# Optimization experiments

Hardware: AMD Instinct MI355X
Metric: run time of the kernel (lower is better)

The kernel has to match this reference:

```python
import jax, jax.numpy as jnp
import numpy as np

N, E, D, C, L, G = 50000, 1600000, 128, 10, 4, 512
BN_EPS = 1e-5


def setup_inputs() -> dict:
    key = jax.random.key(0)
    ks = jax.random.split(key, 16)
    s = 0.05  # weight init scale
    inp = {
        "x": jax.random.normal(ks[0], (N, D), dtype=jnp.float32),
        "edge_index": jax.random.randint(ks[1], (2, E), 0, N, dtype=jnp.int32),
        "batch": jnp.sort(jax.random.randint(ks[2], (N,), 0, G, dtype=jnp.int32)),
        "num_graphs": G,
        # GINConv inner MLP params (layer 0 input dim == D since num_features == num_hidden)
        "conv_W1": jax.random.normal(ks[3], (L, D, D), dtype=jnp.float32) * s,
        "conv_b1": jnp.zeros((L, D), dtype=jnp.float32),
        "conv_bn_g": jnp.ones((L, D), dtype=jnp.float32),
        "conv_bn_b": jnp.zeros((L, D), dtype=jnp.float32),
        "conv_W2": jax.random.normal(ks[4], (L, D, D), dtype=jnp.float32) * s,
        "conv_b2": jnp.zeros((L, D), dtype=jnp.float32),
        # outer BatchNorm after each conv
        "bn_g": jnp.ones((L, D), dtype=jnp.float32),
        "bn_b": jnp.zeros((L, D), dtype=jnp.float32),
        # per-scale classifier heads (L+1 of them; fcs[0] input dim == num_features == D)
        "fc_W": jax.random.normal(ks[5], (L + 1, D, C), dtype=jnp.float32) * s,
        "fc_b": jnp.zeros((L + 1, C), dtype=jnp.float32),
    }
    return inp


def _bn(h, g, b):
    # BatchNorm1d in training mode: batch stats over nodes, biased variance
    m = h.mean(axis=0)
    v = jnp.mean((h - m) ** 2, axis=0)
    return (h - m) * jax.lax.rsqrt(v + BN_EPS) * g + b


def reference(x, edge_index, batch, num_graphs, conv_W1, conv_b1, conv_bn_g,
              conv_bn_b, conv_W2, conv_b2, bn_g, bn_b, fc_W, fc_b):
    n_nodes = x.shape[0]
    src, dst = edge_index[0], edge_index[1]
    outs = [x]
    h = x
    for i in range(L):
        # GINConv (eps=0, aggr='add'): mlp(x + scatter_add of neighbor features)
        agg = jax.ops.segment_sum(h[src], dst, num_segments=n_nodes)  # [N, D]
        z = h + agg
        z = z @ conv_W1[i] + conv_b1[i]
        z = jax.nn.relu(_bn(z, conv_bn_g[i], conv_bn_b[i]))
        z = z @ conv_W2[i] + conv_b2[i]
        h = jax.nn.relu(_bn(z, bn_g[i], bn_b[i]))
        outs.append(h)
    out = None
    for i, o in enumerate(outs):
        pooled = jax.ops.segment_sum(o, batch, num_segments=num_graphs)  # [G, D]
        logits = pooled @ fc_W[i] + fc_b[i]
        out = logits if out is None else out + logits
    return jax.nn.log_softmax(out, axis=-1)
```

## Files before the change

kernel.cpp:

```cpp
#include <hip/hip_runtime.h>

#define NN 50000
#define EE 1600000
#define DD 128
#define CC 10
#define LLAY 4
#define GG 512
#define GD (GG*DD)
#define NB 196
#define BK_EDGES 1024
#define BUCKCAP 16000
#define NSUB 16
#define SUBW 3125
#define WPAD 136

static constexpr float BN_EPS = 1e-5f;
static constexpr float INV_N = 1.0f / (float)NN;

typedef __bf16 bf16x8 __attribute__((ext_vector_type(8)));
typedef float f32x4 __attribute__((ext_vector_type(4)));

static __device__ __forceinline__ float bflo(unsigned u){ return __uint_as_float(u << 16); }
static __device__ __forceinline__ float bfhi(unsigned u){ return __uint_as_float(u & 0xffff0000u); }
static __device__ __forceinline__ unsigned short f2bf(float f){
    unsigned u = __float_as_uint(f);
    return (unsigned short)((u + 0x7fffu + ((u >> 16) & 1u)) >> 16);
}
static __device__ __forceinline__ unsigned packbf(float a, float b){
    return (unsigned)f2bf(a) | ((unsigned)f2bf(b) << 16);
}
static __device__ __forceinline__ unsigned encf(float f){
    unsigned b = __float_as_uint(f);
    return (b & 0x80000000u) ? ~b : (b | 0x80000000u);
}
static __device__ __forceinline__ float decf(unsigned e){
    unsigned b = (e & 0x80000000u) ? (e ^ 0x80000000u) : ~e;
    return __uint_as_float(b);
}
static __device__ __forceinline__ bf16x8 ldfrag(const unsigned short* p){
    union { uint4 u; bf16x8 b; } t; t.u = *(const uint4*)p; return t.b;
}
static __device__ __forceinline__ bf16x8 asfrag(uint4 u){
    union { uint4 u; bf16x8 b; } t; t.u = u; return t.b;
}


__global__ void zero_k(int* p, int n){
    int i = blockIdx.x * 256 + threadIdx.x;
    if (i < n) p[i] = 0;
}

__global__ void wprep_k(const float* __restrict__ W1, const float* __restrict__ W2,
                        unsigned short* __restrict__ Wtall){
    int idx = blockIdx.x * 256 + threadIdx.x;
    int mat = idx >> 14; int rr = idx & 16383;
    int k = rr >> 7; int j = rr & 127;
    const float* Wsrc = (mat < 4) ? (W1 + mat * 16384) : (W2 + (mat - 4) * 16384);
    Wtall[mat * 16384 + j * 128 + k] = f2bf(Wsrc[k * 128 + j]);
}

__global__ void gsearch_k(const int* __restrict__ batch, int* __restrict__ gstart){
    int g = blockIdx.x * 256 + threadIdx.x;
    if (g <= GG){
        int lo = 0, hi = NN;
        while (lo < hi){ int mid = (lo + hi) >> 1; if (batch[mid] < g) lo = mid + 1; else hi = mid; }
        gstart[g] = lo;
    }
}

__global__ __launch_bounds__(256) void binA_k(const int* __restrict__ srcA,
                                              const int* __restrict__ dstA,
                                              int* __restrict__ bucketCur,
                                              unsigned* __restrict__ binned){
    __shared__ int cnt[256];
    __shared__ int lb[256];
    __shared__ int bas[NB];
    __shared__ int off[NB];
    __shared__ unsigned stage[BK_EDGES];
    __shared__ int tots;
    int tid = threadIdx.x;
    cnt[tid] = 0;
    if (tid < NB) off[tid] = 0;
    __syncthreads();
    int e0 = blockIdx.x * BK_EDGES;
    int myB[4]; unsigned myVal[4];
    #pragma unroll
    for (int k = 0; k < 4; k++){
        int e = e0 + tid + k * 256;
        bool v = (e < EE);
        int d = v ? dstA[e] : -1;
        int s = v ? srcA[e] : 0;
        myB[k] = v ? (d >> 8) : -1;
        myVal[k] = (unsigned)s | ((unsigned)(d & 255) << 17);
        if (v) atomicAdd(&cnt[d >> 8], 1);
    }
    __syncthreads();
    int v = cnt[tid];
    lb[tid] = v; __syncthreads();
    for (int o = 1; o < 256; o <<= 1){
        int x = 0; if (tid >= o) x = lb[tid - o];
        __syncthreads(); lb[tid] += x; __syncthreads();
    }
    int incl = lb[tid];
    if (tid == 255) tots = incl;
    __syncthreads();
    lb[tid] = incl - v;
    if (tid < NB && v > 0) bas[tid] = atomicAdd(&bucketCur[tid], v);
    __syncthreads();
    #pragma unroll
    for (int k = 0; k < 4; k++){
        int b = myB[k];
        if (b >= 0){
            int p = lb[b] + atomicAdd(&off[b], 1);
            stage[p] = myVal[k];
        }
    }
    __syncthreads();
    int tot = tots;
    for (int i = tid; i < tot; i += 256){
        int lo = 0, hi = NB - 1;
        while (lo < hi){
            int mid = (lo + hi + 1) >> 1;
            if (lb[mid] <= i) lo = mid; else hi = mid - 1;
        }
        binned[lo * BUCKCAP + bas[lo] + (i - lb[lo])] = stage[i];
    }
}

__global__ __launch_bounds__(256) void bscan_k(const int* __restrict__ bucketCur,
                                               int* __restrict__ bucketBase,
                                               int* __restrict__ rp){
    __shared__ int lds[256];
    int t = threadIdx.x;
    int v = (t < NB) ? bucketCur[t] : 0;
    lds[t] = v; __syncthreads();
    for (int o = 1; o < 256; o <<= 1){
        int xv = 0; if (t >= o) xv = lds[t - o];
        __syncthreads(); lds[t] += xv; __syncthreads();
    }
    int excl = lds[t] - v;
    if (t < NB) bucketBase[t] = excl;
    if (t == 0){ bucketBase[NB] = EE; rp[NN] = EE; }
}

__global__ __launch_bounds__(1024) void binB_k(const unsigned* __restrict__ binned,
                                               const int* __restrict__ bucketCur,
                                               const int* __restrict__ bucketBase,
                                               int* __restrict__ rp,
                                               int* __restrict__ ssort){
    __shared__ int c16[256 * NSUB];
    __shared__ int b16[256 * NSUB];
    __shared__ int nt[256];
    int b = blockIdx.x, tid = threadIdx.x;
    int nb0 = b * 256;
    int nmax = NN - nb0; if (nmax > 256) nmax = 256;
    for (int i = tid; i < 256 * NSUB; i += 1024) c16[i] = 0;
    __syncthreads();
    int cntb = bucketCur[b];
    int src0 = b * BUCKCAP;
    int base = bucketBase[b];
    for (int i = tid; i < cntb; i += 1024){
        unsigned u = binned[src0 + i];
        int src = (int)(u & 0x1FFFFu); int dl = (int)(u >> 17);
        atomicAdd(&c16[dl * NSUB + src / SUBW], 1);
    }
    __syncthreads();
    int cc[NSUB]; int tot = 0;
    if (tid < 256){
        #pragma unroll
        for (int k = 0; k < NSUB; k++){ cc[k] = c16[tid * NSUB + k]; tot += cc[k]; }
        nt[tid] = tot;
    }
    __syncthreads();
    for (int o = 1; o < 256; o <<= 1){
        int xv = 0;
        if (tid < 256 && tid >= o) xv = nt[tid - o];
        __syncthreads();
        if (tid < 256) nt[tid] += xv;
        __syncthreads();
    }
    if (tid < 256){
        int p = base + nt[tid] - tot;
        if (tid < nmax) rp[nb0 + tid] = p;
        int run = p;
        #pragma unroll
        for (int k = 0; k < NSUB; k++){ b16[tid * NSUB + k] = run; run += cc[k]; }
    }
    __syncthreads();
    for (int i = tid; i < 256 * NSUB; i += 1024) c16[i] = 0;
    __syncthreads();
    for (int i = tid; i < cntb; i += 1024){
        unsigned u = binned[src0 + i];
        int src = (int)(u & 0x1FFFFu); int dl = (int)(u >> 17);
        int t = src / SUBW;
        int pos = b16[dl * NSUB + t] + atomicAdd(&c16[dl * NSUB + t], 1);
        ssort[pos] = src;
    }
}

__global__ __launch_bounds__(256) void xmax_k(const float* __restrict__ x,
                                              unsigned* __restrict__ xmaxE){
    __shared__ float sm[256];
    int tid = threadIdx.x;
    int col = tid & 127, rh = tid >> 7;
    float m = 0.f;
    for (int r = blockIdx.x * 2 + rh; r < NN; r += 1024)
        m = fmaxf(m, fabsf(x[r * 128 + col]));
    sm[tid] = m; __syncthreads();
    if (tid < 128){
        m = fmaxf(sm[tid], sm[tid + 128]);
        atomicMax(&xmaxE[col], __float_as_uint(m));
    }
}

__global__ void qx_k(const unsigned* __restrict__ xmaxE,
                     float* __restrict__ qD, float* __restrict__ qR){
    int c = threadIdx.x;
    float m = __uint_as_float(xmaxE[c]);
    qD[c] = m * (1.f / 127.f);
    qR[c] = (m > 0.f) ? 127.f / m : 0.f;
}

__global__ __launch_bounds__(256) void convxpool_k(const float2* __restrict__ x2,
                                                   const int* __restrict__ gstart,
                                                   unsigned short* __restrict__ h8u,
                                                   const float* __restrict__ qR0,
                                                   float* __restrict__ outp){
    __shared__ float sd[512];
    int b = blockIdx.x; int gid = b >> 2, chunk = b & 3;
    int tid = threadIdx.x; int c = tid & 63, rs = tid >> 6;
    int s = gstart[gid], e = gstart[gid + 1];
    float2 rv = ((const float2*)qR0)[c];
    float a0 = 0.f, a1 = 0.f;
    for (int n = s + chunk * 4 + rs; n < e; n += 16){
        float2 v = x2[n * 64 + c];
        int i0 = (int)rintf(v.x * rv.x) + 128; i0 = min(max(i0, 0), 255);
        int i1 = (int)rintf(v.y * rv.y) + 128; i1 = min(max(i1, 0), 255);
        h8u[n * 64 + c] = (unsigned short)(i0 | (i1 << 8));
        a0 += v.x; a1 += v.y;
    }
    sd[tid] = a0; sd[256 + tid] = a1; __syncthreads();
    if (tid < 64){
        float r0 = 0.f, r1 = 0.f;
        #pragma unroll
        for (int k2 = 0; k2 < 4; k2++){ r0 += sd[tid + 64 * k2]; r1 += sd[256 + tid + 64 * k2]; }
        atomicAdd(&outp[gid * 128 + 2 * tid], r0);
        atomicAdd(&outp[gid * 128 + 2 * tid + 1], r1);
    }
}


__global__ __launch_bounds__(256) void agg_k(const unsigned short* __restrict__ h8u,
                                             const int* __restrict__ rp,
                                             const int* __restrict__ ssort,
                                             const float* __restrict__ qD,
                                             float offv,
                                             unsigned* __restrict__ z32,
                                             float* __restrict__ zstats){
    int tid = threadIdx.x;
    if (blockIdx.x == 0) zstats[tid] = 0.f;
    int n = blockIdx.x * 4 + (tid >> 6);
    int lane = tid & 63;
    int e  = __builtin_amdgcn_readfirstlane(rp[n]);
    int e1 = __builtin_amdgcn_readfirstlane(rp[n + 1]);
    int deg = e1 - e;
    unsigned su = (unsigned)h8u[n * 64 + lane];
    unsigned acc0 = su & 0xFFu, acc1 = su >> 8;
    for (; e + 15 < e1; e += 16){
        int sA[16];
        #pragma unroll
        for (int k = 0; k < 16; k++) sA[k] = ssort[e + k];
        unsigned uA[16];
        #pragma unroll
        for (int k = 0; k < 16; k++) uA[k] = (unsigned)h8u[sA[k] * 64 + lane];
        #pragma unroll
        for (int k = 0; k < 16; k++){ acc0 += uA[k] & 0xFFu; acc1 += uA[k] >> 8; }
    }
    for (; e + 3 < e1; e += 4){
        int s0 = ssort[e], s1 = ssort[e + 1], s2 = ssort[e + 2], s3 = ssort[e + 3];
        unsigned u0 = (unsigned)h8u[s0 * 64 + lane];
        unsigned u1 = (unsigned)h8u[s1 * 64 + lane];
        unsigned u2 = (unsigned)h8u[s2 * 64 + lane];
        unsigned u3 = (unsigned)h8u[s3 * 64 + lane];
        acc0 += (u0 & 0xFFu) + (u1 & 0xFFu) + (u2 & 0xFFu) + (u3 & 0xFFu);
        acc1 += (u0 >> 8) + (u1 >> 8) + (u2 >> 8) + (u3 >> 8);
    }
    for (; e < e1; ++e){
        unsigned u0 = (unsigned)h8u[ssort[e] * 64 + lane];
        acc0 += u0 & 0xFFu; acc1 += u0 >> 8;
    }
    float2 qd = ((const float2*)qD)[lane];
    float degoff = offv * (float)(deg + 1);
    float z0 = qd.x * ((float)acc0 - degoff);
    float z1 = qd.y * ((float)acc1 - degoff);
    z32[n * 64 + lane] = packbf(z0, z1);
}

template<int TR>
__global__ __launch_bounds__(256) void gemm_k(const unsigned* __restrict__ A32,
                                              const unsigned short* __restrict__ Wtg,
                                              const float* __restrict__ bias,
                                              unsigned short* __restrict__ Cst,
                                              const float* __restrict__ stats,
                                              const float* __restrict__ gma,
                                              const float* __restrict__ bta,
                                              float* __restrict__ ostats,
                                              float* __restrict__ zstats,
                                              float* __restrict__ zpool,
                                              unsigned* __restrict__ mst){
    __shared__ __align__(16) unsigned short Wl[64 * WPAD];
    __shared__ float sred[1024];
    __shared__ __align__(16) float sl[128], tl[128];
    int tid = threadIdx.x;
    int slice = blockIdx.x & 1;
    int tileb = blockIdx.x >> 1;

    int wv = tid >> 6, lane = tid & 63;
    int rowbase = tileb * 64 + wv * 16;
    int r0 = rowbase + (lane & 15);
    int kd = (lane >> 4) * 4;
    uint4 va[4];
    #pragma unroll
    for (int ks = 0; ks < 4; ks++)
        va[ks] = (r0 < NN) ? *(const uint4*)(A32 + r0 * 64 + ks * 16 + kd) : make_uint4(0,0,0,0);

    if (blockIdx.x == 0 && zstats) zstats[tid] = 0.f;
    if (zpool && blockIdx.x < 256) zpool[blockIdx.x * 256 + tid] = 0.f;
    {
        const uint4* src = (const uint4*)(Wtg + slice * 64 * 128);
        uint4* dst = (uint4*)Wl;
        #pragma unroll
        for (int i = 0; i < 4; i++){
            int idx = tid + 256 * i;
            int row = idx >> 4, c16 = idx & 15;
            dst[row * (WPAD / 8) + c16] = src[idx];
        }
    }
    if (TR && tid < 128){
        float mean = stats[tid] * INV_N;
        float q    = stats[128 + tid] * INV_N;
        float inv  = rsqrtf(q - mean * mean + BN_EPS);
        float s    = gma[tid] * inv;
        sl[tid] = s; tl[tid] = bta[tid] - mean * s;
    }
    __syncthreads();

    if (TR){
        #pragma unroll
        for (int ks = 0; ks < 4; ks++){
            int q = ks * 8 + (lane >> 4) * 2;
            float4 sA = ((const float4*)sl)[q], sB = ((const float4*)sl)[q + 1];
            float4 tA = ((const float4*)tl)[q], tB = ((const float4*)tl)[q + 1];
            float fs[8] = {sA.x, sA.y, sA.z, sA.w, sB.x, sB.y, sB.z, sB.w};
            float ft[8] = {tA.x, tA.y, tA.z, tA.w, tB.x, tB.y, tB.z, tB.w};
            unsigned* pa = (unsigned*)&va[ks];
            #pragma unroll
            for (int c = 0; c < 4; c++){
                float f0 = fmaxf(bflo(pa[c]) * fs[2*c] + ft[2*c], 0.f);
                float f1 = fmaxf(bfhi(pa[c]) * fs[2*c+1] + ft[2*c+1], 0.f);
                pa[c] = packbf(f0, f1);
            }
        }
    }

    f32x4 acc[4];
    #pragma unroll
    for (int ct = 0; ct < 4; ct++) acc[ct] = (f32x4){0.f, 0.f, 0.f, 0.f};

    #pragma unroll
    for (int ks = 0; ks < 4; ks++){
        int wk = ks * 32 + (lane >> 4) * 8;
        bf16x8 a0 = asfrag(va[ks]);
        #pragma unroll
        for (int ct = 0; ct < 4; ++ct){
            bf16x8 b = ldfrag(&Wl[(ct * 16 + (lane & 15)) * WPAD + wk]);
            acc[ct] = __builtin_amdgcn_mfma_f32_16x16x32_bf16(a0, b, acc[ct], 0, 0, 0);
        }
    }

    int cl = lane & 15, rq = lane >> 4;
    float colS[4], colQ[4];
    #pragma unroll
    for (int ct = 0; ct < 4; ++ct){
        int col = slice * 64 + ct * 16 + cl;
        float bv = bias[col];
        float ps = 0.f, pq = 0.f;
        float vx = -3.4e38f, vn = -3.4e38f;
        #pragma unroll
        for (int rr2 = 0; rr2 < 4; ++rr2){
            int grow = rowbase + rq * 4 + rr2;
            if (grow < NN){
                float val = acc[ct][rr2] + bv;
                Cst[grow * 128 + col] = f2bf(val);
                ps += val; pq += val * val;
                if (TR){ vx = fmaxf(vx, val); vn = fmaxf(vn, -val); }
            }
        }
        ps += __shfl_xor(ps, 16); pq += __shfl_xor(pq, 16);
        ps += __shfl_xor(ps, 32); pq += __shfl_xor(pq, 32);
        colS[ct] = ps; colQ[ct] = pq;
        if (TR){
            vx = fmaxf(vx, __shfl_xor(vx, 16)); vx = fmaxf(vx, __shfl_xor(vx, 32));
            vn = fmaxf(vn, __shfl_xor(vn, 16)); vn = fmaxf(vn, __shfl_xor(vn, 32));
            if (rq == 0){
                sred[512 + wv * 64 + ct * 16 + cl] = vx;
                sred[768 + wv * 64 + ct * 16 + cl] = vn;
            }
        }
    }
    if (rq == 0){
        #pragma unroll
        for (int ct = 0; ct < 4; ++ct){
            sred[wv * 64 + ct * 16 + cl]       = colS[ct];
            sred[256 + wv * 64 + ct * 16 + cl] = colQ[ct];
        }
    }
    __syncthreads();
    if (tid < 64){
        float s1 = sred[tid] + sred[64 + tid] + sred[128 + tid] + sred[192 + tid];
        float s2 = sred[256 + tid] + sred[320 + tid] + sred[384 + tid] + sred[448 + tid];
        atomicAdd(&ostats[slice * 64 + tid], s1);
        atomicAdd(&ostats[128 + slice * 64 + tid], s2);
        if (TR){
            float mx = fmaxf(fmaxf(sred[512 + tid], sred[576 + tid]),
                             fmaxf(sred[640 + tid], sred[704 + tid]));
            float mn = fmaxf(fmaxf(sred[768 + tid], sred[832 + tid]),
                             fmaxf(sred[896 + tid], sred[960 + tid]));
            atomicMax(&mst[slice * 64 + tid], encf(mx));
            atomicMax(&mst[128 + slice * 64 + tid], encf(mn));
        }
    }
}

__global__ __launch_bounds__(256) void ewpool_k(const unsigned* __restrict__ z32,
                                                const float* __restrict__ stats,
                                                const float* __restrict__ g,
                                                const float* __restrict__ b,
                                                const int* __restrict__ gstart,
                                                unsigned short* __restrict__ h8u,
                                                const unsigned* __restrict__ mst,
                                                float* __restrict__ qDn,
                                                float* __restrict__ outp){
    __shared__ float sd[512];
    int blk = blockIdx.x; int gid = blk >> 2, chunk = blk & 3;
    int tid = threadIdx.x;
    int c = tid & 63, rs = tid >> 6;
    int c2 = c * 2;
    float m0 = stats[c2] * INV_N,     q0 = stats[128 + c2] * INV_N;
    float inv0 = rsqrtf(q0 - m0 * m0 + BN_EPS);
    float s0 = g[c2] * inv0, t0 = b[c2] - m0 * s0;
    float m1 = stats[c2 + 1] * INV_N, q1 = stats[129 + c2] * INV_N;
    float inv1 = rsqrtf(q1 - m1 * m1 + BN_EPS);
    float s1 = g[c2 + 1] * inv1, t1 = b[c2 + 1] - m1 * s1;
    float zx0 = decf(mst[c2]),      zn0 = -decf(mst[128 + c2]);
    float zx1 = decf(mst[c2 + 1]),  zn1 = -decf(mst[129 + c2]);
    float hm0 = fmaxf(fmaxf(s0 * zx0 + t0, s0 * zn0 + t0), 0.f);
    float hm1 = fmaxf(fmaxf(s1 * zx1 + t1, s1 * zn1 + t1), 0.f);
    float r80 = (hm0 > 0.f) ? 255.f / hm0 : 0.f;
    float r81 = (hm1 > 0.f) ? 255.f / hm1 : 0.f;
    if (blk == 0 && rs == 0){
        qDn[c2]     = hm0 * (1.f / 255.f);
        qDn[c2 + 1] = hm1 * (1.f / 255.f);
    }
    int s = gstart[gid], e = gstart[gid + 1];
    float a0 = 0.f, a1 = 0.f;
    int n = s + chunk * 4 + rs;
    for (; n + 16 < e; n += 32){
        unsigned u0 = z32[n * 64 + c];
        unsigned u1 = z32[(n + 16) * 64 + c];
        float f0 = fmaxf(bflo(u0) * s0 + t0, 0.f);
        float f1 = fmaxf(bfhi(u0) * s1 + t1, 0.f);
        unsigned cu0 = (unsigned)(f0 * r80 + 0.5f); if (cu0 > 255u) cu0 = 255u;
        unsigned cu1 = (unsigned)(f1 * r81 + 0.5f); if (cu1 > 255u) cu1 = 255u;
        h8u[n * 64 + c] = (unsigned short)(cu0 | (cu1 << 8));
        a0 += f0; a1 += f1;
        f0 = fmaxf(bflo(u1) * s0 + t0, 0.f);
        f1 = fmaxf(bfhi(u1) * s1 + t1, 0.f);
        cu0 = (unsigned)(f0 * r80 + 0.5f); if (cu0 > 255u) cu0 = 255u;
        cu1 = (unsigned)(f1 * r81 + 0.5f); if (cu1 > 255u) cu1 = 255u;
        h8u[(n + 16) * 64 + c] = (unsigned short)(cu0 | (cu1 << 8));
        a0 += f0; a1 += f1;
    }
    for (; n < e; n += 16){
        unsigned u = z32[n * 64 + c];
        float f0 = fmaxf(bflo(u) * s0 + t0, 0.f);
        float f1 = fmaxf(bfhi(u) * s1 + t1, 0.f);
        unsigned cu0 = (unsigned)(f0 * r80 + 0.5f); if (cu0 > 255u) cu0 = 255u;
        unsigned cu1 = (unsigned)(f1 * r81 + 0.5f); if (cu1 > 255u) cu1 = 255u;
        h8u[n * 64 + c] = (unsigned short)(cu0 | (cu1 << 8));
        a0 += f0; a1 += f1;
    }
    sd[tid] = a0; sd[256 + tid] = a1; __syncthreads();
    if (tid < 64){
        float r0 = 0.f, r1 = 0.f;
        #pragma unroll
        for (int k2 = 0; k2 < 4; k2++){ r0 += sd[tid + 64 * k2]; r1 += sd[256 + tid + 64 * k2]; }
        atomicAdd(&outp[gid * 128 + 2 * tid], r0);
        atomicAdd(&outp[gid * 128 + 2 * tid + 1], r1);
    }
}

__global__ __launch_bounds__(64) void final_k(const float* __restrict__ pooled,
                                              const float* __restrict__ fcW,
                                              const float* __restrict__ fcb,
                                              float* __restrict__ out){
    int g = blockIdx.x, l = threadIdx.x;
    float p0[5], p1[5];
    #pragma unroll
    for (int i = 0; i < 5; i++){
        p0[i] = pooled[i * GD + g * 128 + l];
        p1[i] = pooled[i * GD + g * 128 + 64 + l];
    }
    float lg[10];
    #pragma unroll
    for (int c2 = 0; c2 < 10; c2++){
        float s = 0;
        #pragma unroll
        for (int i = 0; i < 5; i++){
            s += p0[i] * fcW[(i * 128 + l) * 10 + c2];
            s += p1[i] * fcW[(i * 128 + 64 + l) * 10 + c2];
        }
        #pragma unroll
        for (int off = 32; off >= 1; off >>= 1) s += __shfl_down(s, off);
        lg[c2] = s;
    }
    if (l == 0){
        #pragma unroll
        for (int c2 = 0; c2 < 10; c2++){
            float bs = 0;
            #pragma unroll
            for (int i = 0; i < 5; i++) bs += fcb[i * 10 + c2];
            lg[c2] += bs;
        }
        float mx = lg[0];
        #pragma unroll
        for (int c2 = 1; c2 < 10; c2++) mx = fmaxf(mx, lg[c2]);
        float se = 0;
        #pragma unroll
        for (int c2 = 0; c2 < 10; c2++) se += expf(lg[c2] - mx);
        float lse = mx + logf(se);
        #pragma unroll
        for (int c2 = 0; c2 < 10; c2++) out[g * 10 + c2] = lg[c2] - lse;
    }
}


extern "C" void kernel_launch(void* const* d_in, const int* in_sizes, int n_in,
                              void* d_out, int out_size, void* d_ws, size_t ws_size,
                              hipStream_t stream){
    (void)in_sizes; (void)n_in; (void)out_size; (void)ws_size;
    const float* x     = (const float*)d_in[0];
    const int*   ei    = (const int*)d_in[1];
    const int*   batch = (const int*)d_in[2];
    const float* cW1   = (const float*)d_in[4];
    const float* cb1   = (const float*)d_in[5];
    const float* cbng  = (const float*)d_in[6];
    const float* cbnb  = (const float*)d_in[7];
    const float* cW2   = (const float*)d_in[8];
    const float* cb2   = (const float*)d_in[9];
    const float* bng   = (const float*)d_in[10];
    const float* bnb   = (const float*)d_in[11];
    const float* fcW   = (const float*)d_in[12];
    const float* fcb   = (const float*)d_in[13];

    char* base = (char*)d_ws;
    size_t off = 0;
    auto alloc = [&](size_t bytes) -> void* {
        void* p = base + off;
        off = (off + bytes + 255) & ~(size_t)255;
        return p;
    };
    unsigned*       zA     = (unsigned*)alloc((size_t)NN * 64 * 4);
    unsigned*       zB     = (unsigned*)alloc((size_t)NN * 64 * 4);
    unsigned short* h8     = (unsigned short*)alloc((size_t)NN * 64 * 2);
    unsigned short* Wtall  = (unsigned short*)alloc(8 * 16384 * 2);
    int*            ssort  = (int*)alloc((size_t)EE * 4);
    int*            rp     = (int*)alloc((NN + 1) * 4);
    int*            gstart = (int*)alloc((GG + 1) * 4);
    int*            bucketBase = (int*)alloc((NB + 1) * 4);
    int*            bucketCur  = (int*)alloc(NB * 4);
    unsigned*       xmaxE  = (unsigned*)alloc(128 * 4);
    unsigned*       mstats = (unsigned*)alloc((size_t)LLAY * 256 * 4);
    float*          pooled = (float*)alloc((size_t)5 * GD * 4);
    float*          stats1 = (float*)alloc(256 * 4);
    float*          stats2 = (float*)alloc(256 * 4);
    float*          qD     = (float*)alloc(5 * 128 * 4);
    float*          qR     = (float*)alloc(128 * 4);
    unsigned*       binned = (unsigned*)zB;

    int zwords = (int)(((char*)(pooled + GD) - (char*)bucketCur) / 4);

    zero_k<<<(zwords + 255) / 256, 256, 0, stream>>>(bucketCur, zwords);
    wprep_k<<<512, 256, 0, stream>>>(cW1, cW2, Wtall);
    gsearch_k<<<3, 256, 0, stream>>>(batch, gstart);
    binA_k<<<(EE + BK_EDGES - 1) / BK_EDGES, 256, 0, stream>>>(ei, ei + EE, bucketCur, binned);
    bscan_k<<<1, 256, 0, stream>>>(bucketCur, bucketBase, rp);
    binB_k<<<NB, 1024, 0, stream>>>(binned, bucketCur, bucketBase, rp, ssort);
    xmax_k<<<512, 256, 0, stream>>>(x, xmaxE);
    qx_k<<<1, 128, 0, stream>>>(xmaxE, qD, qR);
    convxpool_k<<<4 * GG, 256, 0, stream>>>((const float2*)x, gstart, h8, qR, pooled);

    const int gemmGrid = 2 * ((NN + 63) / 64);
    for (int i = 0; i < LLAY; i++){
        agg_k<<<NN / 4, 256, 0, stream>>>(h8, rp, ssort,
                                          qD + i * 128, (i == 0) ? 128.f : 0.f, zA, stats1);
        gemm_k<0><<<gemmGrid, 256, 0, stream>>>(zA, Wtall + i * 16384, cb1 + i * 128,
                                                (unsigned short*)zB,
                                                nullptr, nullptr, nullptr, stats1, stats2,
                                                nullptr, nullptr);
        gemm_k<1><<<gemmGrid, 256, 0, stream>>>(zB, Wtall + (4 + i) * 16384, cb2 + i * 128,
                                                (unsigned short*)zA,
                                                stats1, cbng + i * 128, cbnb + i * 128, stats2,
                                                nullptr, pooled + (size_t)(i + 1) * GD,
                                                mstats + (size_t)i * 256);
        ewpool_k<<<4 * GG, 256, 0, stream>>>(zA, stats2, bng + i * 128, bnb + i * 128,
                                             gstart, h8, mstats + (size_t)i * 256,
                                             qD + (i + 1) * 128,
                                             pooled + (size_t)(i + 1) * GD);
    }
    final_k<<<GG, 64, 0, stream>>>(pooled, fcW, fcb, (float*)d_out);
}
```

Before: 604.9 us.

## Double GEMM rows per wave and spread BN stat atomics over slots

Each GEMM wave now computes two 16-row tiles (128 rows per block), so every LDS weight fragment feeds two MFMAs and the grid is half as large. The BN sum, sum-of-squares and max atomics are spread across 8 slots chosen by tile index, and consumers add or max-reduce across the slots. This cuts atomic contention on the same 256 addresses. The stats buffers are now per layer and rely on the upfront zero kernel instead of in-kernel zeroing, which depends on the zero range still covering them. Register pressure per thread rises.

Result: faster. 507.7 us (-16.1%).

```diff
diff --git a/kernel.cpp b/kernel.cpp
--- a/kernel.cpp
+++ b/kernel.cpp
@@ -13,6 +13,7 @@
 #define NSUB 16
 #define SUBW 3125
 #define WPAD 136
+#define NSLOT 8
 
 static constexpr float BN_EPS = 1e-5f;
 static constexpr float INV_N = 1.0f / (float)NN;
@@ -255,10 +256,8 @@
                                              const int* __restrict__ ssort,
                                              const float* __restrict__ qD,
                                              float offv,
-                                             unsigned* __restrict__ z32,
-                                             float* __restrict__ zstats){
+                                             unsigned* __restrict__ z32){
     int tid = threadIdx.x;
-    if (blockIdx.x == 0) zstats[tid] = 0.f;
     int n = blockIdx.x * 4 + (tid >> 6);
     int lane = tid & 63;
     int e  = __builtin_amdgcn_readfirstlane(rp[n]);
@@ -305,7 +304,6 @@
                                               const float* __restrict__ gma,
                                               const float* __restrict__ bta,
                                               float* __restrict__ ostats,
-                                              float* __restrict__ zstats,
                                               float* __restrict__ zpool,
                                               unsigned* __restrict__ mst){
     __shared__ __align__(16) unsigned short Wl[64 * WPAD];
@@ -314,17 +312,20 @@
     int tid = threadIdx.x;
     int slice = blockIdx.x & 1;
     int tileb = blockIdx.x >> 1;
+    int slot = tileb & (NSLOT - 1);
 
     int wv = tid >> 6, lane = tid & 63;
-    int rowbase = tileb * 64 + wv * 16;
+    int rowbase = tileb * 128 + wv * 32;
     int r0 = rowbase + (lane & 15);
+    int r1 = r0 + 16;
     int kd = (lane >> 4) * 4;
-    uint4 va[4];
-    #pragma unroll
-    for (int ks = 0; ks < 4; ks++)
+    uint4 va[4], vb[4];
+    #pragma unroll
+    for (int ks = 0; ks < 4; ks++){
         va[ks] = (r0 < NN) ? *(const uint4*)(A32 + r0 * 64 + ks * 16 + kd) : make_uint4(0,0,0,0);
-
-    if (blockIdx.x == 0 && zstats) zstats[tid] = 0.f;
+        vb[ks] = (r1 < NN) ? *(const uint4*)(A32 + r1 * 64 + ks * 16 + kd) : make_uint4(0,0,0,0);
+    }
+
     if (zpool && blockIdx.x < 256) zpool[blockIdx.x * 256 + tid] = 0.f;
     {
         const uint4* src = (const uint4*)(Wtg + slice * 64 * 128);
@@ -337,8 +338,14 @@
         }
     }
     if (TR && tid < 128){
-        float mean = stats[tid] * INV_N;
-        float q    = stats[128 + tid] * INV_N;
+        float sum1 = 0.f, sum2 = 0.f;
+        #pragma unroll
+        for (int s8 = 0; s8 < NSLOT; s8++){
+            sum1 += stats[s8 * 256 + tid];
+            sum2 += stats[s8 * 256 + 128 + tid];
+        }
+        float mean = sum1 * INV_N;
+        float q    = sum2 * INV_N;
         float inv  = rsqrtf(q - mean * mean + BN_EPS);
         float s    = gma[tid] * inv;
         sl[tid] = s; tl[tid] = bta[tid] - mean * s;
@@ -354,27 +361,35 @@
             float fs[8] = {sA.x, sA.y, sA.z, sA.w, sB.x, sB.y, sB.z, sB.w};
             float ft[8] = {tA.x, tA.y, tA.z, tA.w, tB.x, tB.y, tB.z, tB.w};
             unsigned* pa = (unsigned*)&va[ks];
+            unsigned* pb = (unsigned*)&vb[ks];
             #pragma unroll
             for (int c = 0; c < 4; c++){
                 float f0 = fmaxf(bflo(pa[c]) * fs[2*c] + ft[2*c], 0.f);
                 float f1 = fmaxf(bfhi(pa[c]) * fs[2*c+1] + ft[2*c+1], 0.f);
                 pa[c] = packbf(f0, f1);
+                f0 = fmaxf(bflo(pb[c]) * fs[2*c] + ft[2*c], 0.f);
+                f1 = fmaxf(bfhi(pb[c]) * fs[2*c+1] + ft[2*c+1], 0.f);
+                pb[c] = packbf(f0, f1);
             }
         }
     }
 
-    f32x4 acc[4];
-    #pragma unroll
-    for (int ct = 0; ct < 4; ct++) acc[ct] = (f32x4){0.f, 0.f, 0.f, 0.f};
+    f32x4 acc[2][4];
+    #pragma unroll
+    for (int a = 0; a < 2; a++)
+        #pragma unroll
+        for (int b = 0; b < 4; b++) acc[a][b] = (f32x4){0.f, 0.f, 0.f, 0.f};
 
     #pragma unroll
     for (int ks = 0; ks < 4; ks++){
         int wk = ks * 32 + (lane >> 4) * 8;
         bf16x8 a0 = asfrag(va[ks]);
+        bf16x8 a1 = asfrag(vb[ks]);
         #pragma unroll
         for (int ct = 0; ct < 4; ++ct){
             bf16x8 b = ldfrag(&Wl[(ct * 16 + (lane & 15)) * WPAD + wk]);
-            acc[ct] = __builtin_amdgcn_mfma_f32_16x16x32_bf16(a0, b, acc[ct], 0, 0, 0);
+            acc[0][ct] = __builtin_amdgcn_mfma_f32_16x16x32_bf16(a0, b, acc[0][ct], 0, 0, 0);
+            acc[1][ct] = __builtin_amdgcn_mfma_f32_16x16x32_bf16(a1, b, acc[1][ct], 0, 0, 0);
         }
     }
 
@@ -387,13 +402,16 @@
         float ps = 0.f, pq = 0.f;
         float vx = -3.4e38f, vn = -3.4e38f;
         #pragma unroll
-        for (int rr2 = 0; rr2 < 4; ++rr2){
-            int grow = rowbase + rq * 4 + rr2;
-            if (grow < NN){
-                float val = acc[ct][rr2] + bv;
-                Cst[grow * 128 + col] = f2bf(val);
-                ps += val; pq += val * val;
-                if (TR){ vx = fmaxf(vx, val); vn = fmaxf(vn, -val); }
+        for (int rt = 0; rt < 2; ++rt){
+            #pragma unroll
+            for (int rr2 = 0; rr2 < 4; ++rr2){
+                int grow = rowbase + rt * 16 + rq * 4 + rr2;
+                if (grow < NN){
+                    float val = acc[rt][ct][rr2] + bv;
+                    Cst[grow * 128 + col] = f2bf(val);
+                    ps += val; pq += val * val;
+                    if (TR){ vx = fmaxf(vx, val); vn = fmaxf(vn, -val); }
+                }
             }
         }
         ps += __shfl_xor(ps, 16); pq += __shfl_xor(pq, 16);
@@ -419,15 +437,15 @@
     if (tid < 64){
         float s1 = sred[tid] + sred[64 + tid] + sred[128 + tid] + sred[192 + tid];
         float s2 = sred[256 + tid] + sred[320 + tid] + sred[384 + tid] + sred[448 + tid];
-        atomicAdd(&ostats[slice * 64 + tid], s1);
-        atomicAdd(&ostats[128 + slice * 64 + tid], s2);
+        atomicAdd(&ostats[slot * 256 + slice * 64 + tid], s1);
+        atomicAdd(&ostats[slot * 256 + 128 + slice * 64 + tid], s2);
         if (TR){
             float mx = fmaxf(fmaxf(sred[512 + tid], sred[576 + tid]),
                              fmaxf(sred[640 + tid], sred[704 + tid]));
             float mn = fmaxf(fmaxf(sred[768 + tid], sred[832 + tid]),
                              fmaxf(sred[896 + tid], sred[960 + tid]));
-            atomicMax(&mst[slice * 64 + tid], encf(mx));
-            atomicMax(&mst[128 + slice * 64 + tid], encf(mn));
+            atomicMax(&mst[slot * 256 + slice * 64 + tid], encf(mx));
+            atomicMax(&mst[slot * 256 + 128 + slice * 64 + tid], encf(mn));
         }
     }
 }
@@ -446,14 +464,23 @@
     int tid = threadIdx.x;
     int c = tid & 63, rs = tid >> 6;
     int c2 = c * 2;
-    float m0 = stats[c2] * INV_N,     q0 = stats[128 + c2] * INV_N;
+    float sm0 = 0.f, sq0 = 0.f, sm1 = 0.f, sq1 = 0.f;
+    unsigned ex0 = 0u, en0 = 0u, ex1 = 0u, en1 = 0u;
+    #pragma unroll
+    for (int s8 = 0; s8 < NSLOT; s8++){
+        sm0 += stats[s8 * 256 + c2];       sq0 += stats[s8 * 256 + 128 + c2];
+        sm1 += stats[s8 * 256 + c2 + 1];   sq1 += stats[s8 * 256 + 129 + c2];
+        ex0 = max(ex0, mst[s8 * 256 + c2]);       en0 = max(en0, mst[s8 * 256 + 128 + c2]);
+        ex1 = max(ex1, mst[s8 * 256 + c2 + 1]);   en1 = max(en1, mst[s8 * 256 + 129 + c2]);
+    }
+    float m0 = sm0 * INV_N, q0 = sq0 * INV_N;
     float inv0 = rsqrtf(q0 - m0 * m0 + BN_EPS);
     float s0 = g[c2] * inv0, t0 = b[c2] - m0 * s0;
-    float m1 = stats[c2 + 1] * INV_N, q1 = stats[129 + c2] * INV_N;
+    float m1 = sm1 * INV_N, q1 = sq1 * INV_N;
     float inv1 = rsqrtf(q1 - m1 * m1 + BN_EPS);
     float s1 = g[c2 + 1] * inv1, t1 = b[c2 + 1] - m1 * s1;
-    float zx0 = decf(mst[c2]),      zn0 = -decf(mst[128 + c2]);
-    float zx1 = decf(mst[c2 + 1]),  zn1 = -decf(mst[129 + c2]);
+    float zx0 = decf(ex0), zn0 = -decf(en0);
+    float zx1 = decf(ex1), zn1 = -decf(en1);
     float hm0 = fmaxf(fmaxf(s0 * zx0 + t0, s0 * zn0 + t0), 0.f);
     float hm1 = fmaxf(fmaxf(s1 * zx1 + t1, s1 * zn1 + t1), 0.f);
     float r80 = (hm0 > 0.f) ? 255.f / hm0 : 0.f;
@@ -580,10 +607,10 @@
     int*            bucketBase = (int*)alloc((NB + 1) * 4);
     int*            bucketCur  = (int*)alloc(NB * 4);
     unsigned*       xmaxE  = (unsigned*)alloc(128 * 4);
-    unsigned*       mstats = (unsigned*)alloc((size_t)LLAY * 256 * 4);
+    unsigned*       mstats = (unsigned*)alloc((size_t)LLAY * NSLOT * 256 * 4);
+    float*          stats1 = (float*)alloc((size_t)LLAY * NSLOT * 256 * 4);
+    float*          stats2 = (float*)alloc((size_t)LLAY * NSLOT * 256 * 4);
     float*          pooled = (float*)alloc((size_t)5 * GD * 4);
-    float*          stats1 = (float*)alloc(256 * 4);
-    float*          stats2 = (float*)alloc(256 * 4);
     float*          qD     = (float*)alloc(5 * 128 * 4);
     float*          qR     = (float*)alloc(128 * 4);
     unsigned*       binned = (unsigned*)zB;
@@ -600,21 +627,24 @@
     qx_k<<<1, 128, 0, stream>>>(xmaxE, qD, qR);
     convxpool_k<<<4 * GG, 256, 0, stream>>>((const float2*)x, gstart, h8, qR, pooled);
 
-    const int gemmGrid = 2 * ((NN + 63) / 64);
+    const int gemmGrid = 2 * ((NN + 127) / 128);
+    const int SL = NSLOT * 256;
     for (int i = 0; i < LLAY; i++){
         agg_k<<<NN / 4, 256, 0, stream>>>(h8, rp, ssort,
-                                          qD + i * 128, (i == 0) ? 128.f : 0.f, zA, stats1);
+                                          qD + i * 128, (i == 0) ? 128.f : 0.f, zA);
         gemm_k<0><<<gemmGrid, 256, 0, stream>>>(zA, Wtall + i * 16384, cb1 + i * 128,
                                                 (unsigned short*)zB,
-                                                nullptr, nullptr, nullptr, stats1, stats2,
-                                                nullptr, nullptr);
+                                                nullptr, nullptr, nullptr,
+                                                stats1 + (size_t)i * SL, nullptr, nullptr);
         gemm_k<1><<<gemmGrid, 256, 0, stream>>>(zB, Wtall + (4 + i) * 16384, cb2 + i * 128,
                                                 (unsigned short*)zA,
-                                                stats1, cbng + i * 128, cbnb + i * 128, stats2,
-                                                nullptr, pooled + (size_t)(i + 1) * GD,
-                                                mstats + (size_t)i * 256);
-        ewpool_k<<<4 * GG, 256, 0, stream>>>(zA, stats2, bng + i * 128, bnb + i * 128,
-                                             gstart, h8, mstats + (size_t)i * 256,
+                                                stats1 + (size_t)i * SL, cbng + i * 128, cbnb + i * 128,
+                                                stats2 + (size_t)i * SL,
+                                                pooled + (size_t)(i + 1) * GD,
+                                                mstats + (size_t)i * SL);
+        ewpool_k<<<4 * GG, 256, 0, stream>>>(zA, stats2 + (size_t)i * SL,
+                                             bng + i * 128, bnb + i * 128,
+                                             gstart, h8, mstats + (size_t)i * SL,
                                              qD + (i + 1) * 128,
                                              pooled + (size_t)(i + 1) * GD);
     }
```
